# Optimization experiments

Measured on AMD Instinct MI355X. Metric: run time of the kernel, lower is better.

Reference implementation:

```python
import jax, jax.numpy as jnp
import numpy as np

N = 50000      # nodes
E = 800000     # message-passing edges
EF = 1000000   # decoder (full) edges
IN = 128       # in_channels
H = 64         # hidden_channels
OUT = 1        # out_channels
T = 128        # num_timesteps
RESCALE = 4000.0  # SinusoidalPosEmb rescale_steps


def sinusoidal_pos_emb(t, dim, num_steps):
    # t: [N] int -> [N, dim]
    x = t.astype(jnp.float32) * (RESCALE / num_steps)
    half = dim // 2
    freqs = jnp.exp(jnp.arange(half, dtype=jnp.float32) * (-jnp.log(10000.0) / (half - 1)))
    ang = x[:, None] * freqs[None, :]            # [N, half]
    return jnp.concatenate([jnp.sin(ang), jnp.cos(ang)], axis=-1)


def gcn_conv(h, W, b, row, col, norm, n):
    # standard GCNConv: linear -> gather src -> scale by sym norm -> scatter-add to dst -> +bias
    x = h @ W                                     # [N, H]
    msg = x[row] * norm[:, None]                  # [E+N, H]
    out = jax.ops.segment_sum(msg, col, num_segments=n)
    return out + b


def setup_inputs() -> dict:
    key = jax.random.key(0)
    ks = jax.random.split(key, 12)
    rn = lambda k, shape, s=0.02: jax.random.normal(k, shape, jnp.float32) * s
    return {
        "x": jax.random.normal(ks[0], (N, IN), jnp.float32),
        "edge_index": jax.random.randint(ks[1], (2, E), 0, N, jnp.int32),
        "full_edge_index": jax.random.randint(ks[2], (2, EF), 0, N, jnp.int32),
        "time_steps": jax.random.randint(ks[3], (N,), 0, T, jnp.int32),
        "W_in": rn(ks[4], (IN, H)), "b_in": jnp.zeros((H,), jnp.float32),
        "W_t1": rn(ks[5], (H, 4 * H)), "b_t1": jnp.zeros((4 * H,), jnp.float32),
        "W_t2": rn(ks[6], (4 * H, H)), "b_t2": jnp.zeros((H,), jnp.float32),
        "W_c0": rn(ks[7], (H, H)), "b_c0": jnp.zeros((H,), jnp.float32),
        "W_c1": rn(ks[8], (H, H)), "b_c1": jnp.zeros((H,), jnp.float32),
        "W_d1": rn(ks[9], (2 * H, H)), "b_d1": jnp.zeros((H,), jnp.float32),
        "W_d2": rn(ks[10], (H, OUT)), "b_d2": jnp.zeros((OUT,), jnp.float32),
    }


def reference(x, edge_index, full_edge_index, time_steps,
              W_in, b_in, W_t1, b_t1, W_t2, b_t2,
              W_c0, b_c0, W_c1, b_c1, W_d1, b_d1, W_d2, b_d2):
    n = x.shape[0]
    # --- embedder (dropout is identity in eval mode) ---
    h = x @ W_in + b_in                                        # [N, H]
    pe = sinusoidal_pos_emb(time_steps, H, T)                  # [N, H]
    t_emb = jax.nn.silu(pe @ W_t1 + b_t1) @ W_t2 + b_t2        # [N, H]
    h_embed = h + t_emb

    # --- GCN encoder: add self-loops once, symmetric normalization ---
    loops = jnp.arange(n, dtype=edge_index.dtype)
    row = jnp.concatenate([edge_index[0], loops])              # [E+N]
    col = jnp.concatenate([edge_index[1], loops])
    deg = jax.ops.segment_sum(jnp.ones_like(col, jnp.float32), col, num_segments=n)
    dinv = jnp.where(deg > 0, jax.lax.rsqrt(deg), 0.0)
    norm = dinv[row] * dinv[col]                               # [E+N]

    h = gcn_conv(h_embed, W_c0, b_c0, row, col, norm, n)
    h = jax.nn.relu(h)                                         # act between layers; norm=None -> identity
    h_enc = gcn_conv(h, W_c1, b_c1, row, col, norm, n)

    # --- edge decoder: gather src/dst, concat, 2-layer SiLU MLP ---
    src, dst = full_edge_index[0], full_edge_index[1]
    feat = jnp.concatenate([h_enc[src], h_enc[dst]], axis=-1)  # [EF, 2H]
    edge_logits = jax.nn.silu(feat @ W_d1 + b_d1) @ W_d2 + b_d2  # [EF, OUT]
    return edge_logits, h_embed, h_enc
```

## Files before the change

kernel.cpp:

```cpp
#include <hip/hip_runtime.h>
#include <hip/hip_bf16.h>
#include <math.h>

#define N_NODES 50000
#define E_MSG   800000
#define E_FULL  1000000
#define IN_C    128
#define H_C     64
#define T_STEPS 128

#define OFF_Win   0
#define OFF_bin   8192
#define OFF_Wt1   8256
#define OFF_bt1   24640
#define OFF_Wt2   24896
#define OFF_bt2   41280
#define OFF_Wc0   41344
#define OFF_bc0   45440
#define OFF_Wc1   45504
#define OFF_bc1   49600
#define OFF_Wd1   49664
#define OFF_bd1   57856
#define OFF_Wd2   57920
#define OFF_bd2   57984
#define W_TOTAL   57985
#define OFF_BSUM  58016
#define OFF_BCUR  58272
#define OFF_FWD1  58624
#define OFF_FWIN  60672
#define OFF_FWC0  64768
#define OFF_TEMB  66816
#define OFF_DINV  75008
#define OFF_CNT   125008
#define OFF_PTR   175008
#define OFF_ELIST 225010
#define OFF_TMP   1025010
#define OFF_TMP2  1025012
#define OFF_ZBF   2625012
#define OFF_ZBF2  4225012
#define OFF_HENC8 5825012

#define OFF_FWC1  OFF_TMP2

#define SCAN_NB   ((N_NODES + 255) / 256)
#define BF_NB     196
#define BF_CH     ((E_MSG + BF_NB - 1) / BF_NB)

typedef __attribute__((ext_vector_type(8))) short bf16x8;
typedef __attribute__((ext_vector_type(4))) float f32x4;

static __device__ __forceinline__ float bf2f(unsigned short u) {
    return __uint_as_float(((unsigned)u) << 16);
}
static __device__ __forceinline__ unsigned short f2bf(float f) {
    unsigned u = __float_as_uint(f);
    unsigned r = (u + 0x7fffu + ((u >> 16) & 1u)) >> 16;
    return (unsigned short)r;
}
static __device__ __forceinline__ unsigned char f2fp8(float f) {
    unsigned u = __float_as_uint(f);
    unsigned s = (u >> 24) & 0x80;
    float a = fminf(__uint_as_float(u & 0x7FFFFFFF), 448.0f);
    if (a < 0.015625f) {
        int qi = (int)rintf(a * 512.0f);
        return (unsigned char)(s | qi);
    }
    unsigned ua = __float_as_uint(a);
    int e = (int)((ua >> 23) & 0xFF) - 127;
    unsigned man = (ua & 0x7FFFFF) | 0x800000;
    unsigned r = man >> 20;
    unsigned rem = man & 0xFFFFF;
    if (rem > 0x80000u || (rem == 0x80000u && (r & 1))) r++;
    if (r == 16) { r = 8; e++; }
    if (e > 8) return (unsigned char)(s | 0x7E);
    return (unsigned char)(s | ((unsigned)(e + 7) << 3) | (r & 7));
}
static __device__ __forceinline__ bool detect_f32(const unsigned short* w, int* scnt) {
    if (threadIdx.x == 0) *scnt = 0;
    __syncthreads();
    int big = 0;
    for (int i = threadIdx.x; i < 2048; i += blockDim.x)
        if (fabsf(bf2f(w[2 * i])) > 0.5f) big++;
    atomicAdd(scnt, big);
    __syncthreads();
    return *scnt > 64;
}

struct CvtArgs { const void* src[14]; };

__global__ void k_cvt(CvtArgs a, float* ws) {
    __shared__ int scnt;
    bool f32 = detect_f32((const unsigned short*)a.src[0], &scnt);
    int t = blockIdx.x * 256 + threadIdx.x;
    if (t >= W_TOTAL) return;
    const int starts[14] = {OFF_Win, OFF_bin, OFF_Wt1, OFF_bt1, OFF_Wt2, OFF_bt2,
                            OFF_Wc0, OFF_bc0, OFF_Wc1, OFF_bc1, OFF_Wd1, OFF_bd1,
                            OFF_Wd2, OFF_bd2};
    int seg = 0;
#pragma unroll
    for (int i = 1; i < 14; i++)
        if (t >= starts[i]) seg = i;
    int off = t - starts[seg];
    ws[t] = f32 ? ((const float*)a.src[seg])[off]
                : bf2f(((const unsigned short*)a.src[seg])[off]);
}

__global__ void __launch_bounds__(256) k_prep(float* ws) {
    int idx = blockIdx.x * 256 + threadIdx.x;
    int local, j, lane, ct, c, t, m, q;
    if (idx < 8192) {
        local = idx;
        j = local & 7; lane = (local >> 3) & 63; ct = local >> 9;
        c = ct >> 2; t = ct & 3; m = lane & 15; q = lane >> 4;
        ((unsigned char*)(ws + OFF_FWD1))[local] =
            f2fp8(16.0f * ws[OFF_Wd1 + (32 * c + 8 * q + j) * 64 + 16 * t + m]);
    } else if (idx < 16384) {
        local = idx - 8192;
        j = local & 7; lane = (local >> 3) & 63; ct = local >> 9;
        c = ct >> 2; t = ct & 3; m = lane & 15; q = lane >> 4;
        ((unsigned short*)(ws + OFF_FWIN))[local] =
            f2bf(ws[OFF_Win + (32 * c + 8 * q + j) * 64 + 16 * t + m]);
    } else if (idx < 20480) {
        local = idx - 16384;
        j = local & 7; lane = (local >> 3) & 63; ct = local >> 9;
        c = ct >> 2; t = ct & 3; m = lane & 15; q = lane >> 4;
        ((unsigned short*)(ws + OFF_FWC0))[local] =
            f2bf(ws[OFF_Wc0 + (32 * c + 8 * q + j) * 64 + 16 * t + m]);
    } else if (idx < 24576) {
        local = idx - 20480;
        j = local & 7; lane = (local >> 3) & 63; ct = local >> 9;
        c = ct >> 2; t = ct & 3; m = lane & 15; q = lane >> 4;
        ((unsigned short*)(ws + OFF_FWC1))[local] =
            f2bf(ws[OFF_Wc1 + (32 * c + 8 * q + j) * 64 + 16 * t + m]);
    }
}

__global__ void __launch_bounds__(64) k_temb(float* ws) {
    const float* Wt1 = ws + OFF_Wt1;
    const float* bt1 = ws + OFF_bt1;
    const float* Wt2 = ws + OFF_Wt2;
    const float* bt2 = ws + OFF_bt2;
    float* temb = ws + OFF_TEMB;
    int t = blockIdx.x;
    int j = threadIdx.x;

    __shared__ float pe[64];
    __shared__ float us[256];

    float xt = (float)t * (4000.0f / 128.0f);
    float sc = -logf(10000.0f) / 31.0f;
    int idx = j & 31;
    float fr = __expf((float)idx * sc);
    float ang = xt * fr;
    pe[j] = (j < 32) ? sinf(ang) : cosf(ang);
    __syncthreads();

    float u[4];
#pragma unroll
    for (int q = 0; q < 4; q++) u[q] = bt1[q * 64 + j];
    for (int k = 0; k < 64; k++) {
        float p = pe[k];
#pragma unroll
        for (int q = 0; q < 4; q++)
            u[q] = fmaf(p, Wt1[k * 256 + q * 64 + j], u[q]);
    }
#pragma unroll
    for (int q = 0; q < 4; q++) {
        float uu = u[q];
        us[q * 64 + j] = uu * __builtin_amdgcn_rcpf(1.0f + __expf(-uu));
    }
    __syncthreads();

    float acc = bt2[j];
    for (int k = 0; k < 256; k++)
        acc = fmaf(us[k], Wt2[k * 64 + j], acc);
    temb[t * 64 + j] = acc;
}

__global__ void __launch_bounds__(256) k_embed(const void* __restrict__ xraw,
                                               const unsigned short* __restrict__ wdet,
                                               const int* __restrict__ tsteps,
                                               float* __restrict__ ws,
                                               float* __restrict__ out_hembed,
                                               unsigned short* __restrict__ zbf) {
    __shared__ int scnt;
    __shared__ unsigned short tl[4][16 * 64];
    bool f32 = detect_f32(wdet, &scnt);

    int lane = threadIdx.x & 63;
    int wv = threadIdx.x >> 6;
    int m = lane & 15, quad = lane >> 4;
    int wid = blockIdx.x * 4 + wv;
    if (wid > N_NODES / 16 - 1) wid = N_NODES / 16 - 1;
    int n0 = wid * 16;

    const unsigned short* fwin = (const unsigned short*)(ws + OFF_FWIN);
    const unsigned short* fwc0 = (const unsigned short*)(ws + OFF_FWC0);

    bf16x8 bI[4][4];
#pragma unroll
    for (int c = 0; c < 4; c++)
#pragma unroll
        for (int t = 0; t < 4; t++)
            bI[c][t] = *reinterpret_cast<const bf16x8*>(fwin + (c * 4 + t) * 512 + lane * 8);

    f32x4 acc[4] = {f32x4{0,0,0,0}, f32x4{0,0,0,0}, f32x4{0,0,0,0}, f32x4{0,0,0,0}};
#pragma unroll
    for (int c = 0; c < 4; c++) {
        bf16x8 a;
        if (f32) {
            const float* xp = (const float*)xraw + (size_t)(n0 + m) * 128 + 32 * c + 8 * quad;
            float4 v0 = *reinterpret_cast<const float4*>(xp);
            float4 v1 = *reinterpret_cast<const float4*>(xp + 4);
            a[0] = (short)f2bf(v0.x); a[1] = (short)f2bf(v0.y);
            a[2] = (short)f2bf(v0.z); a[3] = (short)f2bf(v0.w);
            a[4] = (short)f2bf(v1.x); a[5] = (short)f2bf(v1.y);
            a[6] = (short)f2bf(v1.z); a[7] = (short)f2bf(v1.w);
        } else {
            a = *reinterpret_cast<const bf16x8*>(
                (const unsigned short*)xraw + (size_t)(n0 + m) * 128 + 32 * c + 8 * quad);
        }
#pragma unroll
        for (int t = 0; t < 4; t++)
            acc[t] = __builtin_amdgcn_mfma_f32_16x16x32_bf16(a, bI[c][t], acc[t], 0, 0, 0);
    }

    int tn[4];
#pragma unroll
    for (int r = 0; r < 4; r++) tn[r] = tsteps[n0 + 4 * quad + r];
    const float* temb = ws + OFF_TEMB;
#pragma unroll
    for (int t = 0; t < 4; t++) {
        int ch = 16 * t + m;
        float bj = ws[OFF_bin + ch];
#pragma unroll
        for (int r = 0; r < 4; r++) {
            int node = n0 + 4 * quad + r;
            float v = acc[t][r] + bj + temb[tn[r] * 64 + ch];
            out_hembed[(size_t)node * 64 + ch] = v;
            tl[wv][(4 * quad + r) * 64 + ch] = f2bf(v);
        }
    }
    __syncthreads();

    bf16x8 bC[2][4];
#pragma unroll
    for (int c = 0; c < 2; c++)
#pragma unroll
        for (int t = 0; t < 4; t++)
            bC[c][t] = *reinterpret_cast<const bf16x8*>(fwc0 + (c * 4 + t) * 512 + lane * 8);

    f32x4 az[4] = {f32x4{0,0,0,0}, f32x4{0,0,0,0}, f32x4{0,0,0,0}, f32x4{0,0,0,0}};
#pragma unroll
    for (int c = 0; c < 2; c++) {
        bf16x8 a2 = *reinterpret_cast<const bf16x8*>(&tl[wv][m * 64 + 32 * c + 8 * quad]);
#pragma unroll
        for (int t = 0; t < 4; t++)
            az[t] = __builtin_amdgcn_mfma_f32_16x16x32_bf16(a2, bC[c][t], az[t], 0, 0, 0);
    }
    const float* dinv = ws + OFF_DINV;
    float dv[4];
#pragma unroll
    for (int r = 0; r < 4; r++) dv[r] = dinv[n0 + 4 * quad + r];
#pragma unroll
    for (int t = 0; t < 4; t++) {
        int ch = 16 * t + m;
#pragma unroll
        for (int r = 0; r < 4; r++)
            zbf[(size_t)(n0 + 4 * quad + r) * 64 + ch] = f2bf(az[t][r] * dv[r]);
    }
}

__global__ void k_count(const int* __restrict__ col, int* __restrict__ cnt) {
    int t = blockIdx.x * 256 + threadIdx.x;
    if (t < E_MSG) atomicAdd(&cnt[col[t]], 1);
}

__global__ void __launch_bounds__(256) k_scan1(const int* __restrict__ cnt,
                                               int* __restrict__ bsum) {
    __shared__ int s[256];
    int n = blockIdx.x * 256 + threadIdx.x;
    s[threadIdx.x] = (n < N_NODES) ? cnt[n] : 0;
    __syncthreads();
    for (int off = 128; off > 0; off >>= 1) {
        if (threadIdx.x < off) s[threadIdx.x] += s[threadIdx.x + off];
        __syncthreads();
    }
    if (threadIdx.x == 0) bsum[blockIdx.x] = s[0];
}

__global__ void __launch_bounds__(256) k_scan2(int* __restrict__ bsum,
                                               int* __restrict__ bcur,
                                               int* __restrict__ ptr) {
    __shared__ int s[256];
    int t = threadIdx.x;
    int v = (t < SCAN_NB) ? bsum[t] : 0;
    s[t] = v;
    __syncthreads();
    for (int off = 1; off < 256; off <<= 1) {
        int u = (t >= off) ? s[t - off] : 0;
        __syncthreads();
        s[t] += u;
        __syncthreads();
    }
    if (t < SCAN_NB) {
        bsum[t] = s[t] - v;
        bcur[t] = s[t] - v;
    }
    if (t == 0) ptr[N_NODES] = E_MSG;
}

__global__ void __launch_bounds__(256) k_scan3(const int* __restrict__ cnt,
                                               const int* __restrict__ bsum,
                                               int* __restrict__ ptr,
                                               float* __restrict__ dinv) {
    __shared__ int s[256];
    int t = threadIdx.x;
    int n = blockIdx.x * 256 + t;
    int v = (n < N_NODES) ? cnt[n] : 0;
    s[t] = v;
    __syncthreads();
    for (int off = 1; off < 256; off <<= 1) {
        int u = (t >= off) ? s[t - off] : 0;
        __syncthreads();
        s[t] += u;
        __syncthreads();
    }
    if (n < N_NODES) {
        ptr[n] = bsum[blockIdx.x] + s[t] - v;
        dinv[n] = rsqrtf((float)v + 1.0f);
    }
}

__global__ void __launch_bounds__(256) k_bfill(const int* __restrict__ row,
                                               const int* __restrict__ col,
                                               int* __restrict__ bcur,
                                               uint2* __restrict__ tmp) {
    __shared__ int hist[SCAN_NB];
    __shared__ int basew[SCAN_NB];
    int b = blockIdx.x;
    int lo = b * BF_CH;
    int hi = lo + BF_CH; if (hi > E_MSG) hi = E_MSG;
    for (int i = threadIdx.x; i < SCAN_NB; i += 256) hist[i] = 0;
    __syncthreads();
    for (int e = lo + threadIdx.x; e < hi; e += 256)
        atomicAdd(&hist[col[e] >> 8], 1);
    __syncthreads();
    for (int i = threadIdx.x; i < SCAN_NB; i += 256) {
        int c = hist[i];
        basew[i] = (c > 0) ? atomicAdd(&bcur[i], c) : 0;
    }
    __syncthreads();
    for (int i = threadIdx.x; i < SCAN_NB; i += 256) hist[i] = 0;
    __syncthreads();
    for (int e = lo + threadIdx.x; e < hi; e += 256) {
        int src = row[e], c = col[e];
        int bk = c >> 8;
        int off = atomicAdd(&hist[bk], 1);
        tmp[basew[bk] + off] = uint2{(unsigned)src, (unsigned)c};
    }
}

__global__ void __launch_bounds__(256) k_csort(const uint2* __restrict__ tmp,
                                               const int* __restrict__ bsum,
                                               const int* __restrict__ ptr,
                                               int* __restrict__ elist) {
    __shared__ int cur[256];
    int b = blockIdx.x;
    int n = (b << 8) + threadIdx.x;
    cur[threadIdx.x] = (n < N_NODES) ? ptr[n] : 0;
    __syncthreads();
    int start = bsum[b];
    int end = (b == SCAN_NB - 1) ? E_MSG : bsum[b + 1];
    for (int e = start + threadIdx.x; e < end; e += 256) {
        uint2 p = tmp[e];
        int pos = atomicAdd(&cur[p.y & 255], 1);
        elist[pos] = (int)p.x;
    }
}

__global__ void __launch_bounds__(256) k_gather0(const unsigned short* __restrict__ zbf,
                                                 const int* __restrict__ ptr,
                                                 const int* __restrict__ elist,
                                                 const float* __restrict__ ws,
                                                 unsigned short* __restrict__ zout) {
    __shared__ unsigned short tile[16 * 64];
    const float* dinv = ws + OFF_DINV;
    const float* bias = ws + OFF_bc0;
    const unsigned short* fwc1 = (const unsigned short*)(ws + OFF_FWC1);

    int lane = threadIdx.x & 63;
    int wv = threadIdx.x >> 6;
    int g = lane >> 4;
    int cl = lane & 15;
    int n0 = blockIdx.x * 16;

    float4 b4 = *reinterpret_cast<const float4*>(bias + 4 * cl);

#pragma unroll
    for (int snode = 0; snode < 4; snode++) {
        int li = wv * 4 + snode;
        int n = n0 + li;
        int base = ptr[n], end = ptr[n + 1];

        float ws0 = (g == 0) ? 1.0f : 0.0f;
        ushort4 sv = *reinterpret_cast<const ushort4*>(zbf + (size_t)n * 64 + cl * 4);
        float s0 = ws0 * bf2f(sv.x), s1 = ws0 * bf2f(sv.y);
        float s2 = ws0 * bf2f(sv.z), s3 = ws0 * bf2f(sv.w);

        for (int k = base; k < end; k += 8) {
            int e0 = k + g, e1 = k + 4 + g;
            int r0 = elist[min(e0, end - 1)];
            int r1 = elist[min(e1, end - 1)];
            ushort4 v0 = *reinterpret_cast<const ushort4*>(zbf + (size_t)r0 * 64 + cl * 4);
            ushort4 v1 = *reinterpret_cast<const ushort4*>(zbf + (size_t)r1 * 64 + cl * 4);
            float w0 = (e0 < end) ? 1.0f : 0.0f;
            float w1 = (e1 < end) ? 1.0f : 0.0f;
            s0 = fmaf(w0, bf2f(v0.x), s0); s1 = fmaf(w0, bf2f(v0.y), s1);
            s2 = fmaf(w0, bf2f(v0.z), s2); s3 = fmaf(w0, bf2f(v0.w), s3);
            s0 = fmaf(w1, bf2f(v1.x), s0); s1 = fmaf(w1, bf2f(v1.y), s1);
            s2 = fmaf(w1, bf2f(v1.z), s2); s3 = fmaf(w1, bf2f(v1.w), s3);
        }
        s0 += __shfl_xor(s0, 16, 64); s0 += __shfl_xor(s0, 32, 64);
        s1 += __shfl_xor(s1, 16, 64); s1 += __shfl_xor(s1, 32, 64);
        s2 += __shfl_xor(s2, 16, 64); s2 += __shfl_xor(s2, 32, 64);
        s3 += __shfl_xor(s3, 16, 64); s3 += __shfl_xor(s3, 32, 64);

        if (g == 0) {
            float dv = dinv[n];
            float h0 = fmaxf(fmaf(dv, s0, b4.x), 0.0f);
            float h1 = fmaxf(fmaf(dv, s1, b4.y), 0.0f);
            float h2 = fmaxf(fmaf(dv, s2, b4.z), 0.0f);
            float h3 = fmaxf(fmaf(dv, s3, b4.w), 0.0f);
            ushort4 hv;
            hv.x = f2bf(h0); hv.y = f2bf(h1); hv.z = f2bf(h2); hv.w = f2bf(h3);
            int bo = li * 128 + ((cl * 8) ^ ((li & 7) << 4));
            *reinterpret_cast<ushort4*>((char*)tile + bo) = hv;
        }
    }
    __syncthreads();

    int m = lane & 15, q = lane >> 4;
    bf16x8 bB0 = *reinterpret_cast<const bf16x8*>(fwc1 + (0 * 4 + wv) * 512 + lane * 8);
    bf16x8 bB1 = *reinterpret_cast<const bf16x8*>(fwc1 + (1 * 4 + wv) * 512 + lane * 8);

    f32x4 az = f32x4{0, 0, 0, 0};
    {
        int bo0 = m * 128 + ((0 * 64 + q * 16) ^ ((m & 7) << 4));
        bf16x8 a0 = *reinterpret_cast<const bf16x8*>((const char*)tile + bo0);
        az = __builtin_amdgcn_mfma_f32_16x16x32_bf16(a0, bB0, az, 0, 0, 0);
        int bo1 = m * 128 + ((1 * 64 + q * 16) ^ ((m & 7) << 4));
        bf16x8 a1 = *reinterpret_cast<const bf16x8*>((const char*)tile + bo1);
        az = __builtin_amdgcn_mfma_f32_16x16x32_bf16(a1, bB1, az, 0, 0, 0);
    }
    float dv4[4];
#pragma unroll
    for (int r = 0; r < 4; r++) dv4[r] = dinv[n0 + 4 * q + r];
#pragma unroll
    for (int r = 0; r < 4; r++) {
        int node = n0 + 4 * q + r;
        zout[(size_t)node * 64 + 16 * wv + m] = f2bf(az[r] * dv4[r]);
    }
}

__global__ void __launch_bounds__(256) k_gather1(const unsigned short* __restrict__ zbf,
                                                 const int* __restrict__ ptr,
                                                 const int* __restrict__ elist,
                                                 const float* __restrict__ dinv,
                                                 const float* __restrict__ bias,
                                                 unsigned char* __restrict__ henc8,
                                                 float* __restrict__ ofp) {
    int lane = threadIdx.x & 63;
    int n = blockIdx.x * 4 + (threadIdx.x >> 6);
    int g = lane >> 4;
    int cl = lane & 15;
    int base = ptr[n], end = ptr[n + 1];

    float4 b4 = *reinterpret_cast<const float4*>(bias + 4 * cl);

    float ws0 = (g == 0) ? 1.0f : 0.0f;
    ushort4 sv = *reinterpret_cast<const ushort4*>(zbf + (size_t)n * 64 + cl * 4);
    float s0 = ws0 * bf2f(sv.x), s1 = ws0 * bf2f(sv.y);
    float s2 = ws0 * bf2f(sv.z), s3 = ws0 * bf2f(sv.w);

    for (int k = base; k < end; k += 8) {
        int e0 = k + g, e1 = k + 4 + g;
        int r0 = elist[min(e0, end - 1)];
        int r1 = elist[min(e1, end - 1)];
        ushort4 v0 = *reinterpret_cast<const ushort4*>(zbf + (size_t)r0 * 64 + cl * 4);
        ushort4 v1 = *reinterpret_cast<const ushort4*>(zbf + (size_t)r1 * 64 + cl * 4);
        float w0 = (e0 < end) ? 1.0f : 0.0f;
        float w1 = (e1 < end) ? 1.0f : 0.0f;
        s0 = fmaf(w0, bf2f(v0.x), s0); s1 = fmaf(w0, bf2f(v0.y), s1);
        s2 = fmaf(w0, bf2f(v0.z), s2); s3 = fmaf(w0, bf2f(v0.w), s3);
        s0 = fmaf(w1, bf2f(v1.x), s0); s1 = fmaf(w1, bf2f(v1.y), s1);
        s2 = fmaf(w1, bf2f(v1.z), s2); s3 = fmaf(w1, bf2f(v1.w), s3);
    }
    s0 += __shfl_xor(s0, 16, 64); s0 += __shfl_xor(s0, 32, 64);
    s1 += __shfl_xor(s1, 16, 64); s1 += __shfl_xor(s1, 32, 64);
    s2 += __shfl_xor(s2, 16, 64); s2 += __shfl_xor(s2, 32, 64);
    s3 += __shfl_xor(s3, 16, 64); s3 += __shfl_xor(s3, 32, 64);

    float dv = dinv[n];
    float o0 = fmaf(dv, s0, b4.x);
    float o1 = fmaf(dv, s1, b4.y);
    float o2 = fmaf(dv, s2, b4.z);
    float o3 = fmaf(dv, s3, b4.w);

    if (g == 0) {
        float4 ov; ov.x = o0; ov.y = o1; ov.z = o2; ov.w = o3;
        *reinterpret_cast<float4*>(ofp + (size_t)n * 64 + cl * 4) = ov;
    }
    int jc = lane >> 2;
    float a0 = __shfl(o0, jc, 64);
    float a1 = __shfl(o1, jc, 64);
    float a2 = __shfl(o2, jc, 64);
    float a3 = __shfl(o3, jc, 64);
    int sel = lane & 3;
    float mv = (sel == 0) ? a0 : (sel == 1) ? a1 : (sel == 2) ? a2 : a3;
    henc8[(size_t)n * 64 + lane] = f2fp8(16.0f * mv);
}

#define DEC_TPW 4
#define DEC_TILES (E_FULL / 16)

__global__ void __launch_bounds__(256) k_dec(const int* __restrict__ src,
                                             const int* __restrict__ dst,
                                             const unsigned char* __restrict__ h8,
                                             const float* __restrict__ ws,
                                             float* __restrict__ out) {
    int lane = threadIdx.x & 63;
    int wv = threadIdx.x >> 6;
    int m = lane & 15;
    int quad = lane >> 4;

    const unsigned char* fw = (const unsigned char*)(ws + OFF_FWD1);
    long bfr[4][4];
#pragma unroll
    for (int c = 0; c < 4; c++)
#pragma unroll
        for (int t = 0; t < 4; t++)
            bfr[c][t] = *reinterpret_cast<const long*>(fw + ((c * 4 + t) * 512 + lane * 8));

    float w2[4], b1v[4];
#pragma unroll
    for (int t = 0; t < 4; t++) {
        w2[t]  = ws[OFF_Wd2 + 16 * t + m];
        b1v[t] = ws[OFF_bd1 + 16 * t + m];
    }
    float b2 = ws[OFF_bd2];

    int tile0 = (blockIdx.x * 4 + wv) * DEC_TPW;
    int tc = min(tile0, DEC_TILES - 1);
    int s0 = src[tc * 16 + m], d0 = dst[tc * 16 + m];
    tc = min(tile0 + 1, DEC_TILES - 1);
    int s1 = src[tc * 16 + m], d1 = dst[tc * 16 + m];
    long A0[4];
#pragma unroll
    for (int c = 0; c < 4; c++) {
        int row = (c < 2) ? s0 : d0;
        A0[c] = *reinterpret_cast<const long*>(
            h8 + (size_t)row * 64 + (c & 1) * 32 + 8 * quad);
    }

    for (int i = 0; i < DEC_TPW; i++) {
        int tile = tile0 + i;
        int t2 = min(tile0 + i + 2, DEC_TILES - 1);
        int s2 = src[t2 * 16 + m], d2 = dst[t2 * 16 + m];
        long A1[4];
#pragma unroll
        for (int c = 0; c < 4; c++) {
            int row = (c < 2) ? s1 : d1;
            A1[c] = *reinterpret_cast<const long*>(
                h8 + (size_t)row * 64 + (c & 1) * 32 + 8 * quad);
        }
        f32x4 acc[4] = {f32x4{0,0,0,0}, f32x4{0,0,0,0}, f32x4{0,0,0,0}, f32x4{0,0,0,0}};
#pragma unroll
        for (int c = 0; c < 4; c++)
#pragma unroll
            for (int t = 0; t < 4; t++)
                acc[t] = __builtin_amdgcn_mfma_f32_16x16x32_fp8_fp8(A0[c], bfr[c][t], acc[t], 0, 0, 0);
        float sums[4];
#pragma unroll
        for (int r = 0; r < 4; r++) {
            float sv = 0.0f;
#pragma unroll
            for (int t = 0; t < 4; t++) {
                float v = fmaf(acc[t][r], 0.00390625f, b1v[t]);
                float h = v * __builtin_amdgcn_rcpf(1.0f + __expf(-v));
                sv = fmaf(h, w2[t], sv);
            }
#pragma unroll
            for (int msk = 8; msk >= 1; msk >>= 1)
                sv += __shfl_xor(sv, msk, 64);
            sums[r] = sv;
        }
        if (m == 0 && tile < DEC_TILES) {
            int ebase = tile * 16 + 4 * quad;
#pragma unroll
            for (int r = 0; r < 4; r++) out[ebase + r] = sums[r] + b2;
        }
#pragma unroll
        for (int c = 0; c < 4; c++) A0[c] = A1[c];
        s1 = s2; d1 = d2;
    }
}

extern "C" void kernel_launch(void* const* d_in, const int* in_sizes, int n_in,
                              void* d_out, int out_size, void* d_ws, size_t ws_size,
                              hipStream_t stream) {
    if (n_in < 18) return;
    const void* x              = d_in[0];
    const int* edge_index      = (const int*)d_in[1];
    const int* full_edge_index = (const int*)d_in[2];
    const int* tsteps          = (const int*)d_in[3];
    float* ws = (float*)d_ws;
    float* out = (float*)d_out;

    int*   iws   = (int*)d_ws;
    int*   bsum  = iws + OFF_BSUM;
    int*   bcur  = iws + OFF_BCUR;
    int*   cnt   = iws + OFF_CNT;
    int*   ptr   = iws + OFF_PTR;
    int*   elist = iws + OFF_ELIST;
    uint2* tmp   = (uint2*)(iws + OFF_TMP2);
    unsigned short* zbf  = (unsigned short*)(ws + OFF_ZBF);
    unsigned short* zbf2 = (unsigned short*)(ws + OFF_ZBF2);
    unsigned char*  h8   = (unsigned char*)(ws + OFF_HENC8);

    CvtArgs ca;
    for (int i = 0; i < 14; i++) ca.src[i] = d_in[4 + i];

    hipMemsetAsync(cnt, 0, (size_t)N_NODES * 4, stream);
    k_count<<<(E_MSG + 255) / 256, 256, 0, stream>>>(edge_index + E_MSG, cnt);
    k_scan1<<<SCAN_NB, 256, 0, stream>>>(cnt, bsum);
    k_scan2<<<1, 256, 0, stream>>>(bsum, bcur, ptr);
    k_scan3<<<SCAN_NB, 256, 0, stream>>>(cnt, bsum, ptr, ws + OFF_DINV);
    k_bfill<<<BF_NB, 256, 0, stream>>>(edge_index, edge_index + E_MSG, bcur, tmp);
    k_csort<<<SCAN_NB, 256, 0, stream>>>(tmp, bsum, ptr, elist);

    k_cvt<<<(W_TOTAL + 255) / 256, 256, 0, stream>>>(ca, ws);
    k_prep<<<96, 256, 0, stream>>>(ws);
    k_temb<<<T_STEPS, 64, 0, stream>>>(ws);

    k_embed<<<(N_NODES / 16 + 3) / 4, 256, 0, stream>>>(
        x, (const unsigned short*)d_in[4], tsteps, ws, out + E_FULL, zbf);

    k_gather0<<<N_NODES / 16, 256, 0, stream>>>(zbf, ptr, elist, ws, zbf2);

    k_gather1<<<N_NODES / 4, 256, 0, stream>>>(
        zbf2, ptr, elist, ws + OFF_DINV, ws + OFF_bc1, h8,
        out + E_FULL + (size_t)N_NODES * 64);

    int dec_blocks = (DEC_TILES + 4 * DEC_TPW - 1) / (4 * DEC_TPW);
    k_dec<<<dec_blocks, 256, 0, stream>>>(full_edge_index, full_edge_index + E_FULL,
                                          h8, ws, out);
}
```

Baseline: 300.3 us.

## Fuse CSR build into cooperative kernel and merge weight-prep kernels

Replaces the memset plus six CSR-construction kernels (count, three scans, bucket fill, counting sort) with one cooperative-launch kernel that uses grid-wide syncs between phases. The weight conversion, fragment packing and time-embedding MLP kernels are merged into one launch that reads raw inputs directly, packing four timesteps per block. Decoder output stores become one float4 store per lane group. The goal is fewer launches and inter-kernel gaps, in exchange for grid-sync overhead and a bucket-fill phase spread over 196 blocks.

```diff
diff --git a/kernel.cpp b/kernel.cpp
--- a/kernel.cpp
+++ b/kernel.cpp
@@ -1,6 +1,9 @@
 #include <hip/hip_runtime.h>
 #include <hip/hip_bf16.h>
+#include <hip/hip_cooperative_groups.h>
 #include <math.h>
+
+namespace cg = cooperative_groups;
 
 #define N_NODES 50000
 #define E_MSG   800000
@@ -43,8 +46,7 @@
 #define OFF_FWC1  OFF_TMP2
 
 #define SCAN_NB   ((N_NODES + 255) / 256)
-#define BF_NB     196
-#define BF_CH     ((E_MSG + BF_NB - 1) / BF_NB)
+#define BF_CH     ((E_MSG + SCAN_NB - 1) / SCAN_NB)
 
 typedef __attribute__((ext_vector_type(8))) short bf16x8;
 typedef __attribute__((ext_vector_type(4))) float f32x4;
@@ -85,96 +87,194 @@
     __syncthreads();
     return *scnt > 64;
 }
+static __device__ __forceinline__ float ldw(const void* p, int idx, bool f32) {
+    return f32 ? ((const float*)p)[idx] : bf2f(((const unsigned short*)p)[idx]);
+}
+
+__global__ void __launch_bounds__(256) k_csr(const int* __restrict__ row,
+                                             const int* __restrict__ col,
+                                             int* cnt, int* bsum, int* bcur,
+                                             int* ptr, float* dinv,
+                                             uint2* tmp, int* elist) {
+    cg::grid_group grid = cg::this_grid();
+    __shared__ int sh[256];
+    __shared__ int hist[SCAN_NB];
+    __shared__ int basew[SCAN_NB];
+    int b = blockIdx.x, t = threadIdx.x;
+
+    for (int n = b * 256 + t; n < N_NODES; n += SCAN_NB * 256) cnt[n] = 0;
+    __threadfence();
+    grid.sync();
+
+    for (int e = b * 256 + t; e < E_MSG; e += SCAN_NB * 256)
+        atomicAdd(&cnt[col[e]], 1);
+    grid.sync();
+
+    int n = b * 256 + t;
+    int v = (n < N_NODES) ? cnt[n] : 0;
+    sh[t] = v;
+    __syncthreads();
+    for (int off = 128; off > 0; off >>= 1) {
+        if (t < off) sh[t] += sh[t + off];
+        __syncthreads();
+    }
+    if (t == 0) bsum[b] = sh[0];
+    __threadfence();
+    grid.sync();
+
+    if (b == 0) {
+        int vv = (t < SCAN_NB) ? bsum[t] : 0;
+        sh[t] = vv;
+        __syncthreads();
+        for (int off = 1; off < 256; off <<= 1) {
+            int u = (t >= off) ? sh[t - off] : 0;
+            __syncthreads();
+            sh[t] += u;
+            __syncthreads();
+        }
+        if (t < SCAN_NB) { bsum[t] = sh[t] - vv; bcur[t] = sh[t] - vv; }
+        if (t == 0) ptr[N_NODES] = E_MSG;
+        __threadfence();
+    }
+    grid.sync();
+
+    sh[t] = v;
+    __syncthreads();
+    for (int off = 1; off < 256; off <<= 1) {
+        int u = (t >= off) ? sh[t - off] : 0;
+        __syncthreads();
+        sh[t] += u;
+        __syncthreads();
+    }
+    if (n < N_NODES) {
+        ptr[n] = bsum[b] + sh[t] - v;
+        dinv[n] = rsqrtf((float)v + 1.0f);
+    }
+    __threadfence();
+    grid.sync();
+
+    int lo = b * BF_CH;
+    int hi = lo + BF_CH; if (hi > E_MSG) hi = E_MSG;
+    for (int i = t; i < SCAN_NB; i += 256) hist[i] = 0;
+    __syncthreads();
+    for (int e = lo + t; e < hi; e += 256)
+        atomicAdd(&hist[col[e] >> 8], 1);
+    __syncthreads();
+    for (int i = t; i < SCAN_NB; i += 256) {
+        int c = hist[i];
+        basew[i] = (c > 0) ? atomicAdd(&bcur[i], c) : 0;
+    }
+    __syncthreads();
+    for (int i = t; i < SCAN_NB; i += 256) hist[i] = 0;
+    __syncthreads();
+    for (int e = lo + t; e < hi; e += 256) {
+        int src = row[e], c = col[e];
+        int bk = c >> 8;
+        int off = atomicAdd(&hist[bk], 1);
+        tmp[basew[bk] + off] = uint2{(unsigned)src, (unsigned)c};
+    }
+    __threadfence();
+    grid.sync();
+
+    int nn = (b << 8) + t;
+    sh[t] = (nn < N_NODES) ? ptr[nn] : 0;
+    __syncthreads();
+    int start = bsum[b];
+    int end = (b == SCAN_NB - 1) ? E_MSG : bsum[b + 1];
+    for (int e = start + t; e < end; e += 256) {
+        uint2 p = tmp[e];
+        int pos = atomicAdd(&sh[p.y & 255], 1);
+        elist[pos] = (int)p.x;
+    }
+}
+
+#define WP_CVT_NB  227
+#define WP_PREP_NB 96
+#define WP_TEMB_NB 32
 
 struct CvtArgs { const void* src[14]; };
 
-__global__ void k_cvt(CvtArgs a, float* ws) {
+__global__ void __launch_bounds__(256) k_wprep(CvtArgs a, float* ws) {
     __shared__ int scnt;
     bool f32 = detect_f32((const unsigned short*)a.src[0], &scnt);
-    int t = blockIdx.x * 256 + threadIdx.x;
-    if (t >= W_TOTAL) return;
-    const int starts[14] = {OFF_Win, OFF_bin, OFF_Wt1, OFF_bt1, OFF_Wt2, OFF_bt2,
-                            OFF_Wc0, OFF_bc0, OFF_Wc1, OFF_bc1, OFF_Wd1, OFF_bd1,
-                            OFF_Wd2, OFF_bd2};
-    int seg = 0;
-#pragma unroll
-    for (int i = 1; i < 14; i++)
-        if (t >= starts[i]) seg = i;
-    int off = t - starts[seg];
-    ws[t] = f32 ? ((const float*)a.src[seg])[off]
-                : bf2f(((const unsigned short*)a.src[seg])[off]);
-}
-
-__global__ void __launch_bounds__(256) k_prep(float* ws) {
-    int idx = blockIdx.x * 256 + threadIdx.x;
-    int local, j, lane, ct, c, t, m, q;
-    if (idx < 8192) {
-        local = idx;
-        j = local & 7; lane = (local >> 3) & 63; ct = local >> 9;
-        c = ct >> 2; t = ct & 3; m = lane & 15; q = lane >> 4;
-        ((unsigned char*)(ws + OFF_FWD1))[local] =
-            f2fp8(16.0f * ws[OFF_Wd1 + (32 * c + 8 * q + j) * 64 + 16 * t + m]);
-    } else if (idx < 16384) {
-        local = idx - 8192;
-        j = local & 7; lane = (local >> 3) & 63; ct = local >> 9;
-        c = ct >> 2; t = ct & 3; m = lane & 15; q = lane >> 4;
-        ((unsigned short*)(ws + OFF_FWIN))[local] =
-            f2bf(ws[OFF_Win + (32 * c + 8 * q + j) * 64 + 16 * t + m]);
-    } else if (idx < 20480) {
-        local = idx - 16384;
-        j = local & 7; lane = (local >> 3) & 63; ct = local >> 9;
-        c = ct >> 2; t = ct & 3; m = lane & 15; q = lane >> 4;
-        ((unsigned short*)(ws + OFF_FWC0))[local] =
-            f2bf(ws[OFF_Wc0 + (32 * c + 8 * q + j) * 64 + 16 * t + m]);
-    } else if (idx < 24576) {
-        local = idx - 20480;
-        j = local & 7; lane = (local >> 3) & 63; ct = local >> 9;
-        c = ct >> 2; t = ct & 3; m = lane & 15; q = lane >> 4;
-        ((unsigned short*)(ws + OFF_FWC1))[local] =
-            f2bf(ws[OFF_Wc1 + (32 * c + 8 * q + j) * 64 + 16 * t + m]);
-    }
-}
-
-__global__ void __launch_bounds__(64) k_temb(float* ws) {
-    const float* Wt1 = ws + OFF_Wt1;
-    const float* bt1 = ws + OFF_bt1;
-    const float* Wt2 = ws + OFF_Wt2;
-    const float* bt2 = ws + OFF_bt2;
-    float* temb = ws + OFF_TEMB;
-    int t = blockIdx.x;
-    int j = threadIdx.x;
-
-    __shared__ float pe[64];
-    __shared__ float us[256];
-
-    float xt = (float)t * (4000.0f / 128.0f);
-    float sc = -logf(10000.0f) / 31.0f;
-    int idx = j & 31;
-    float fr = __expf((float)idx * sc);
-    float ang = xt * fr;
-    pe[j] = (j < 32) ? sinf(ang) : cosf(ang);
-    __syncthreads();
-
-    float u[4];
-#pragma unroll
-    for (int q = 0; q < 4; q++) u[q] = bt1[q * 64 + j];
-    for (int k = 0; k < 64; k++) {
-        float p = pe[k];
-#pragma unroll
-        for (int q = 0; q < 4; q++)
-            u[q] = fmaf(p, Wt1[k * 256 + q * 64 + j], u[q]);
-    }
-#pragma unroll
-    for (int q = 0; q < 4; q++) {
-        float uu = u[q];
-        us[q * 64 + j] = uu * __builtin_amdgcn_rcpf(1.0f + __expf(-uu));
-    }
-    __syncthreads();
-
-    float acc = bt2[j];
-    for (int k = 0; k < 256; k++)
-        acc = fmaf(us[k], Wt2[k * 64 + j], acc);
-    temb[t * 64 + j] = acc;
+    int bid = blockIdx.x;
+    int tid = threadIdx.x;
+
+    if (bid < WP_CVT_NB) {
+        int t = bid * 256 + tid;
+        if (t >= W_TOTAL) return;
+        const int starts[14] = {OFF_Win, OFF_bin, OFF_Wt1, OFF_bt1, OFF_Wt2, OFF_bt2,
+                                OFF_Wc0, OFF_bc0, OFF_Wc1, OFF_bc1, OFF_Wd1, OFF_bd1,
+                                OFF_Wd2, OFF_bd2};
+        int seg = 0;
+#pragma unroll
+        for (int i = 1; i < 14; i++)
+            if (t >= starts[i]) seg = i;
+        ws[t] = ldw(a.src[seg], t - starts[seg], f32);
+    } else if (bid < WP_CVT_NB + WP_PREP_NB) {
+        int idx = (bid - WP_CVT_NB) * 256 + tid;
+        int local, j, lane, ct, c, t, m, q;
+        if (idx < 8192) {
+            local = idx;
+            j = local & 7; lane = (local >> 3) & 63; ct = local >> 9;
+            c = ct >> 2; t = ct & 3; m = lane & 15; q = lane >> 4;
+            ((unsigned char*)(ws + OFF_FWD1))[local] =
+                f2fp8(16.0f * ldw(a.src[10], (32 * c + 8 * q + j) * 64 + 16 * t + m, f32));
+        } else if (idx < 16384) {
+            local = idx - 8192;
+            j = local & 7; lane = (local >> 3) & 63; ct = local >> 9;
+            c = ct >> 2; t = ct & 3; m = lane & 15; q = lane >> 4;
+            ((unsigned short*)(ws + OFF_FWIN))[local] =
+                f2bf(ldw(a.src[0], (32 * c + 8 * q + j) * 64 + 16 * t + m, f32));
+        } else if (idx < 20480) {
+            local = idx - 16384;
+            j = local & 7; lane = (local >> 3) & 63; ct = local >> 9;
+            c = ct >> 2; t = ct & 3; m = lane & 15; q = lane >> 4;
+            ((unsigned short*)(ws + OFF_FWC0))[local] =
+                f2bf(ldw(a.src[6], (32 * c + 8 * q + j) * 64 + 16 * t + m, f32));
+        } else {
+            local = idx - 20480;
+            j = local & 7; lane = (local >> 3) & 63; ct = local >> 9;
+            c = ct >> 2; t = ct & 3; m = lane & 15; q = lane >> 4;
+            ((unsigned short*)(ws + OFF_FWC1))[local] =
+                f2bf(ldw(a.src[8], (32 * c + 8 * q + j) * 64 + 16 * t + m, f32));
+        }
+    } else {
+        __shared__ float pe[4][64];
+        __shared__ float us[4][256];
+        int g = tid >> 6;
+        int j = tid & 63;
+        int t = (bid - WP_CVT_NB - WP_PREP_NB) * 4 + g;
+
+        float xt = (float)t * (4000.0f / 128.0f);
+        float sc = -logf(10000.0f) / 31.0f;
+        int idx = j & 31;
+        float fr = __expf((float)idx * sc);
+        float ang = xt * fr;
+        pe[g][j] = (j < 32) ? sinf(ang) : cosf(ang);
+        __syncthreads();
+
+        float u[4];
+#pragma unroll
+        for (int q = 0; q < 4; q++) u[q] = ldw(a.src[3], q * 64 + j, f32);
+        for (int k = 0; k < 64; k++) {
+            float p = pe[g][k];
+#pragma unroll
+            for (int q = 0; q < 4; q++)
+                u[q] = fmaf(p, ldw(a.src[2], k * 256 + q * 64 + j, f32), u[q]);
+        }
+#pragma unroll
+        for (int q = 0; q < 4; q++) {
+            float uu = u[q];
+            us[g][q * 64 + j] = uu * __builtin_amdgcn_rcpf(1.0f + __expf(-uu));
+        }
+        __syncthreads();
+
+        float acc = ldw(a.src[5], j, f32);
+        for (int k = 0; k < 256; k++)
+            acc = fmaf(us[g][k], ldw(a.src[4], k * 64 + j, f32), acc);
+        (ws + OFF_TEMB)[t * 64 + j] = acc;
+    }
 }
 
 __global__ void __launch_bounds__(256) k_embed(const void* __restrict__ xraw,
@@ -271,114 +371,6 @@
     }
 }
 
-__global__ void k_count(const int* __restrict__ col, int* __restrict__ cnt) {
-    int t = blockIdx.x * 256 + threadIdx.x;
-    if (t < E_MSG) atomicAdd(&cnt[col[t]], 1);
-}
-
-__global__ void __launch_bounds__(256) k_scan1(const int* __restrict__ cnt,
-                                               int* __restrict__ bsum) {
-    __shared__ int s[256];
-    int n = blockIdx.x * 256 + threadIdx.x;
-    s[threadIdx.x] = (n < N_NODES) ? cnt[n] : 0;
-    __syncthreads();
-    for (int off = 128; off > 0; off >>= 1) {
-        if (threadIdx.x < off) s[threadIdx.x] += s[threadIdx.x + off];
-        __syncthreads();
-    }
-    if (threadIdx.x == 0) bsum[blockIdx.x] = s[0];
-}
-
-__global__ void __launch_bounds__(256) k_scan2(int* __restrict__ bsum,
-                                               int* __restrict__ bcur,
-                                               int* __restrict__ ptr) {
-    __shared__ int s[256];
-    int t = threadIdx.x;
-    int v = (t < SCAN_NB) ? bsum[t] : 0;
-    s[t] = v;
-    __syncthreads();
-    for (int off = 1; off < 256; off <<= 1) {
-        int u = (t >= off) ? s[t - off] : 0;
-        __syncthreads();
-        s[t] += u;
-        __syncthreads();
-    }
-    if (t < SCAN_NB) {
-        bsum[t] = s[t] - v;
-        bcur[t] = s[t] - v;
-    }
-    if (t == 0) ptr[N_NODES] = E_MSG;
-}
-
-__global__ void __launch_bounds__(256) k_scan3(const int* __restrict__ cnt,
-                                               const int* __restrict__ bsum,
-                                               int* __restrict__ ptr,
-                                               float* __restrict__ dinv) {
-    __shared__ int s[256];
-    int t = threadIdx.x;
-    int n = blockIdx.x * 256 + t;
-    int v = (n < N_NODES) ? cnt[n] : 0;
-    s[t] = v;
-    __syncthreads();
-    for (int off = 1; off < 256; off <<= 1) {
-        int u = (t >= off) ? s[t - off] : 0;
-        __syncthreads();
-        s[t] += u;
-        __syncthreads();
-    }
-    if (n < N_NODES) {
-        ptr[n] = bsum[blockIdx.x] + s[t] - v;
-        dinv[n] = rsqrtf((float)v + 1.0f);
-    }
-}
-
-__global__ void __launch_bounds__(256) k_bfill(const int* __restrict__ row,
-                                               const int* __restrict__ col,
-                                               int* __restrict__ bcur,
-                                               uint2* __restrict__ tmp) {
-    __shared__ int hist[SCAN_NB];
-    __shared__ int basew[SCAN_NB];
-    int b = blockIdx.x;
-    int lo = b * BF_CH;
-    int hi = lo + BF_CH; if (hi > E_MSG) hi = E_MSG;
-    for (int i = threadIdx.x; i < SCAN_NB; i += 256) hist[i] = 0;
-    __syncthreads();
-    for (int e = lo + threadIdx.x; e < hi; e += 256)
-        atomicAdd(&hist[col[e] >> 8], 1);
-    __syncthreads();
-    for (int i = threadIdx.x; i < SCAN_NB; i += 256) {
-        int c = hist[i];
-        basew[i] = (c > 0) ? atomicAdd(&bcur[i], c) : 0;
-    }
-    __syncthreads();
-    for (int i = threadIdx.x; i < SCAN_NB; i += 256) hist[i] = 0;
-    __syncthreads();
-    for (int e = lo + threadIdx.x; e < hi; e += 256) {
-        int src = row[e], c = col[e];
-        int bk = c >> 8;
-        int off = atomicAdd(&hist[bk], 1);
-        tmp[basew[bk] + off] = uint2{(unsigned)src, (unsigned)c};
-    }
-}
-
-__global__ void __launch_bounds__(256) k_csort(const uint2* __restrict__ tmp,
-                                               const int* __restrict__ bsum,
-                                               const int* __restrict__ ptr,
-                                               int* __restrict__ elist) {
-    __shared__ int cur[256];
-    int b = blockIdx.x;
-    int n = (b << 8) + threadIdx.x;
-    cur[threadIdx.x] = (n < N_NODES) ? ptr[n] : 0;
-    __syncthreads();
-    int start = bsum[b];
-    int end = (b == SCAN_NB - 1) ? E_MSG : bsum[b + 1];
-    for (int e = start + threadIdx.x; e < end; e += 256) {
-        uint2 p = tmp[e];
-        int pos = atomicAdd(&cur[p.y & 255], 1);
-        elist[pos] = (int)p.x;
-    }
-}
-
 __global__ void __launch_bounds__(256) k_gather0(const unsigned short* __restrict__ zbf,
                                                  const int* __restrict__ ptr,
                                                  const int* __restrict__ elist,
@@ -596,9 +588,10 @@
             sums[r] = sv;
         }
         if (m == 0 && tile < DEC_TILES) {
-            int ebase = tile * 16 + 4 * quad;
-#pragma unroll
-            for (int r = 0; r < 4; r++) out[ebase + r] = sums[r] + b2;
+            float4 o;
+            o.x = sums[0] + b2; o.y = sums[1] + b2;
+            o.z = sums[2] + b2; o.w = sums[3] + b2;
+            *reinterpret_cast<float4*>(out + tile * 16 + 4 * quad) = o;
         }
 #pragma unroll
         for (int c = 0; c < 4; c++) A0[c] = A1[c];
@@ -631,17 +624,18 @@
     CvtArgs ca;
     for (int i = 0; i < 14; i++) ca.src[i] = d_in[4 + i];
 
-    hipMemsetAsync(cnt, 0, (size_t)N_NODES * 4, stream);
-    k_count<<<(E_MSG + 255) / 256, 256, 0, stream>>>(edge_index + E_MSG, cnt);
-    k_scan1<<<SCAN_NB, 256, 0, stream>>>(cnt, bsum);
-    k_scan2<<<1, 256, 0, stream>>>(bsum, bcur, ptr);
-    k_scan3<<<SCAN_NB, 256, 0, stream>>>(cnt, bsum, ptr, ws + OFF_DINV);
-    k_bfill<<<BF_NB, 256, 0, stream>>>(edge_index, edge_index + E_MSG, bcur, tmp);
-    k_csort<<<SCAN_NB, 256, 0, stream>>>(tmp, bsum, ptr, elist);
-
-    k_cvt<<<(W_TOTAL + 255) / 256, 256, 0, stream>>>(ca, ws);
-    k_prep<<<96, 256, 0, stream>>>(ws);
-    k_temb<<<T_STEPS, 64, 0, stream>>>(ws);
+    {
+        const int* row_p = edge_index;
+        const int* col_p = edge_index + E_MSG;
+        float* dinv_p = ws + OFF_DINV;
+        void* args[] = {(void*)&row_p, (void*)&col_p, (void*)&cnt, (void*)&bsum,
+                        (void*)&bcur, (void*)&ptr, (void*)&dinv_p, (void*)&tmp,
+                        (void*)&elist};
+        hipLaunchCooperativeKernel((const void*)k_csr, dim3(SCAN_NB), dim3(256),
+                                   args, 0, stream);
+    }
+
+    k_wprep<<<WP_CVT_NB + WP_PREP_NB + WP_TEMB_NB, 256, 0, stream>>>(ca, ws);
 
     k_embed<<<(N_NODES / 16 + 3) / 4, 256, 0, stream>>>(
         x, (const unsigned short*)d_in[4], tsteps, ws, out + E_FULL, zbf);
```

Measured after the change: 577.4 us. 1.92x slower.
